# Kernel optimization log

Measured on AMD Instinct MI355X. Metric: run time of the kernel, lower is better.

Reference implementation:

```python
import jax, jax.numpy as jnp
import numpy as np

N_EMBD = 1024
N_HEAD = 16
HEAD = N_EMBD // N_HEAD


def setup_inputs() -> dict:
    key = jax.random.key(0)
    ks = jax.random.split(key, 5)
    B, T = 2, 2048
    s = 1.0 / np.sqrt(N_EMBD)
    return {
        "x": jax.random.normal(ks[0], (B, T, N_EMBD), jnp.float32),
        "w_attn": jax.random.normal(ks[1], (N_EMBD, 3 * N_EMBD), jnp.float32) * s,
        "b_attn": jnp.zeros((3 * N_EMBD,), jnp.float32),
        "w_proj": jax.random.normal(ks[2], (N_EMBD, N_EMBD), jnp.float32) * s,
        "b_proj": jnp.zeros((N_EMBD,), jnp.float32),
    }


def reference(x, w_attn, b_attn, w_proj, b_proj):
    B, T, C = x.shape
    qkv = x @ w_attn + b_attn                      # [B,T,3C]
    q, k, v = jnp.split(qkv, 3, axis=-1)
    def heads(t):
        return t.reshape(B, T, N_HEAD, HEAD).transpose(0, 2, 1, 3)  # [B,H,T,D]
    q, k, v = heads(q), heads(k), heads(v)
    scale = 1.0 / np.sqrt(HEAD)
    att = jnp.einsum('bhqd,bhkd->bhqk', q, k) * scale
    causal = jnp.tril(jnp.ones((T, T), bool))
    att = jnp.where(causal, att, -jnp.inf)
    p = jax.nn.softmax(att, axis=-1)
    y = jnp.einsum('bhqk,bhkd->bhqd', p, v)        # [B,H,T,D]
    y = y.transpose(0, 2, 1, 3).reshape(B, T, C)
    return y @ w_proj + b_proj
```

## Files before the change

### kernel.cpp

```cpp
#include <hip/hip_runtime.h>
#include <hip/hip_bf16.h>

typedef __attribute__((ext_vector_type(4))) float f32x4;
typedef __attribute__((ext_vector_type(16))) float f32x16;
typedef __attribute__((ext_vector_type(8))) short bf16x8;
typedef __attribute__((ext_vector_type(4))) unsigned int u32x4;

#define MFMA16(a,b,c) __builtin_amdgcn_mfma_f32_16x16x32_bf16(a,b,c,0,0,0)
#define MFMA32(a,b,c) __builtin_amdgcn_mfma_f32_32x32x16_bf16(a,b,c,0,0,0)
#define LOG2E 1.44269504088896340736f

__device__ __forceinline__ float bf2f(unsigned short u){
  unsigned v = ((unsigned)u) << 16;
  float f; __builtin_memcpy(&f, &v, 4); return f;
}
__device__ __forceinline__ unsigned short f2bf(float f){
  unsigned x; __builtin_memcpy(&x, &f, 4);
  x += 0x7fffu + ((x >> 16) & 1u);
  return (unsigned short)(x >> 16);
}
__device__ __forceinline__ void gload_lds16(const void* g, void* l){
  __builtin_amdgcn_global_load_lds((const __attribute__((address_space(1))) void*)g,
                                   (__attribute__((address_space(3))) void*)l, 16, 0, 0);
}
__device__ __forceinline__ f32x16 zero16(){
  f32x16 z;
#pragma unroll
  for (int i = 0; i < 16; ++i) z[i] = 0.f;
  return z;
}
__device__ __forceinline__ unsigned cvtpk(float lo, float hi_){
  unsigned d;
  asm("v_cvt_pk_bf16_f32 %0, %1, %2" : "=v"(d) : "v"(lo), "v"(hi_));
  return d;
}
__device__ __forceinline__ void pack_group(const float* p, bf16x8& f0, bf16x8& f1){
  unsigned a0 = cvtpk(p[0], p[1]),  b0 = cvtpk(p[4],  p[5]);
  unsigned a1 = cvtpk(p[2], p[3]),  b1 = cvtpk(p[6],  p[7]);
  unsigned c0 = cvtpk(p[8], p[9]),  d0 = cvtpk(p[12], p[13]);
  unsigned c1 = cvtpk(p[10],p[11]), d1 = cvtpk(p[14], p[15]);
  asm("v_permlane32_swap_b32 %0, %1" : "+v"(a0), "+v"(b0));
  asm("v_permlane32_swap_b32 %0, %1" : "+v"(a1), "+v"(b1));
  asm("v_permlane32_swap_b32 %0, %1" : "+v"(c0), "+v"(d0));
  asm("v_permlane32_swap_b32 %0, %1" : "+v"(c1), "+v"(d1));
  u32x4 w0 = {a0, a1, b0, b1};
  u32x4 w1 = {c0, c1, d0, d1};
  f0 = __builtin_bit_cast(bf16x8, w0);
  f1 = __builtin_bit_cast(bf16x8, w1);
}

__global__ void k_cast(const float* __restrict__ src, unsigned short* __restrict__ dst){
  const int i = blockIdx.x * 256 + threadIdx.x;
  const float4 v = ((const float4*)src)[i];
  ushort4 o;
  o.x = f2bf(v.x); o.y = f2bf(v.y); o.z = f2bf(v.z); o.w = f2bf(v.w);
  ((ushort4*)dst)[i] = o;
}

__global__ void k_castT(const float* __restrict__ src, unsigned short* __restrict__ dst,
                        const int R, const int C){
  __shared__ unsigned short t[64][65];
  const int r0 = blockIdx.y * 64, c0 = blockIdx.x * 64;
  const int tid = threadIdx.x;
#pragma unroll
  for (int i = 0; i < 16; ++i){
    int idx = i*256 + tid; int r = idx >> 6, c = idx & 63;
    t[r][c] = f2bf(src[(size_t)(r0 + r)*C + c0 + c]);
  }
  __syncthreads();
#pragma unroll
  for (int i = 0; i < 16; ++i){
    int idx = i*256 + tid; int c = idx >> 6, r = idx & 63;
    dst[(size_t)(c0 + c)*R + r0 + r] = t[r][c];
  }
}

__device__ __forceinline__ void gemm_core3(const unsigned short* __restrict__ A,
                                           const unsigned short* __restrict__ Bt,
                                           const int K, const int bm, const int bn,
                                           char* ldsb, f32x4 acc[4][4])
{
  const int tid = threadIdx.x, lane = tid & 63, wave = tid >> 6;
  const int wr = wave >> 1, wc = wave & 1;
  const int l15 = lane & 15, lg = lane >> 4;
  const int o = tid * 16;
  const int srow = o >> 6;
  const int sch = ((o >> 4) & 3) ^ ((srow >> 1) & 3);
  const unsigned short* gA0 = A  + (size_t)(bm + srow)*K      + sch*8;
  const unsigned short* gA1 = A  + (size_t)(bm + 64 + srow)*K + sch*8;
  const unsigned short* gB0 = Bt + (size_t)(bn + srow)*K      + sch*8;
  const unsigned short* gB1 = Bt + (size_t)(bn + 64 + srow)*K + sch*8;
  const int rsw = (l15 >> 1) & 3;
  const int aoff = (wr*64 + l15)*64 + ((lg ^ rsw) << 4);
  const int boff = 8192 + (wc*64 + l15)*64 + ((lg ^ rsw) << 4);

#define STG3(koff, bb) do { \
    gload_lds16(gA0 + (koff), ldsb + (bb) + o); \
    gload_lds16(gA1 + (koff), ldsb + (bb) + 4096 + o); \
    gload_lds16(gB0 + (koff), ldsb + (bb) + 8192 + o); \
    gload_lds16(gB1 + (koff), ldsb + (bb) + 12288 + o); } while(0)

  const int NT = K >> 5;
  STG3(0, 0);
  STG3(32, 16384);
  int bcur = 0, bstg = 32768;
  for (int t = 0; t < NT; ++t){
    if (t + 1 < NT) asm volatile("s_waitcnt vmcnt(4)" ::: "memory");
    else            asm volatile("s_waitcnt vmcnt(0)" ::: "memory");
    __builtin_amdgcn_s_barrier();
    __builtin_amdgcn_sched_barrier(0);
    if (t + 2 < NT) STG3((size_t)(t + 2) << 5, bstg);
    bf16x8 af[4], bg[4];
#pragma unroll
    for (int m = 0; m < 4; ++m) af[m] = *(const bf16x8*)(ldsb + bcur + aoff + m*1024);
#pragma unroll
    for (int n = 0; n < 4; ++n) bg[n] = *(const bf16x8*)(ldsb + bcur + boff + n*1024);
    __builtin_amdgcn_s_setprio(1);
#pragma unroll
    for (int m = 0; m < 4; ++m)
#pragma unroll
      for (int n = 0; n < 4; ++n)
        acc[m][n] = MFMA16(af[m], bg[n], acc[m][n]);
    __builtin_amdgcn_s_setprio(0);
    bcur = (bcur == 32768) ? 0 : bcur + 16384;
    bstg = (bstg == 32768) ? 0 : bstg + 16384;
  }
#undef STG3
}

__global__ __launch_bounds__(256,3) void k_gemm_qkv(const unsigned short* __restrict__ xb,
    const unsigned short* __restrict__ waT, const float* __restrict__ b_attn,
    unsigned short* __restrict__ qb, unsigned short* __restrict__ kb,
    unsigned short* __restrict__ vb)
{
  __shared__ char lds[49152];
  f32x4 acc[4][4];
#pragma unroll
  for (int m = 0; m < 4; ++m)
#pragma unroll
    for (int n = 0; n < 4; ++n) acc[m][n] = (f32x4){0.f,0.f,0.f,0.f};
  int wgid = blockIdx.y * 24 + blockIdx.x;
  wgid = (wgid & 7) * 96 + (wgid >> 3);
  const int bm = (wgid / 24) * 128, bn = (wgid % 24) * 128;
  gemm_core3(xb, waT, 1024, bm, bn, lds, acc);
  const int lane = threadIdx.x & 63, wave = threadIdx.x >> 6;
  const int wr = wave >> 1, wc = wave & 1, l15 = lane & 15, lg = lane >> 4;
#pragma unroll
  for (int m = 0; m < 4; ++m){
#pragma unroll
    for (int n = 0; n < 4; ++n){
#pragma unroll
      for (int r = 0; r < 4; ++r){
        const int row = bm + wr*64 + m*16 + lg*4 + r;
        const int col = bn + wc*64 + n*16 + l15;
        const float val = acc[m][n][r] + b_attn[col];
        const int part = col >> 10, c = col & 1023;
        const int h = c >> 6, d = c & 63;
        const int b = row >> 11, t = row & 2047;
        const unsigned short u = f2bf(val);
        const size_t bhbase = (size_t)(b*16 + h)*131072;
        if (part == 0){
          qb[bhbase + (size_t)t*64 + d] = u;
        } else {
          const int tile = t >> 6, l = t & 63;
          const size_t base = bhbase + (size_t)tile*4096;
          if (part == 1) kb[base + l*64 + ((((d>>3)^(l&7))<<3) | (d&7))] = u;
          else           vb[base + d*64 + ((((l>>3)^(d&7))<<3) | (l&7))] = u;
        }
      }
    }
  }
}

__device__ __forceinline__ void gemm_core_s(const unsigned short* __restrict__ A,
                                            const unsigned short* __restrict__ Bt,
                                            const int K, const int bm, const int bn,
                                            char* ldsb, f32x4 acc[2][4])
{
  const int tid = threadIdx.x, lane = tid & 63, wave = tid >> 6;
  const int wr = wave >> 1, wc = wave & 1;
  const int l15 = lane & 15, lg = lane >> 4;
  const int o = tid * 16;
  const int srow = o >> 6;
  const int sch = ((o >> 4) & 3) ^ ((srow >> 1) & 3);
  const unsigned short* gA0 = A  + (size_t)(bm + srow)*K      + sch*8;
  const unsigned short* gB0 = Bt + (size_t)(bn + srow)*K      + sch*8;
  const unsigned short* gB1 = Bt + (size_t)(bn + 64 + srow)*K + sch*8;
  const int rsw = (l15 >> 1) & 3;
  const int aoff = (wr*32 + l15)*64 + ((lg ^ rsw) << 4);
  const int boff = 4096 + (wc*64 + l15)*64 + ((lg ^ rsw) << 4);

#define STGS(koff, bb) do { \
    gload_lds16(gA0 + (koff), ldsb + (bb) + o); \
    gload_lds16(gB0 + (koff), ldsb + (bb) + 4096 + o); \
    gload_lds16(gB1 + (koff), ldsb + (bb) + 8192 + o); } while(0)

  const int NT = K >> 5;
  STGS(0, 0);
  STGS(32, 12288);
  int bcur = 0, bstg = 24576;
  for (int t = 0; t < NT; ++t){
    if (t + 1 < NT) asm volatile("s_waitcnt vmcnt(3)" ::: "memory");
    else            asm volatile("s_waitcnt vmcnt(0)" ::: "memory");
    __builtin_amdgcn_s_barrier();
    __builtin_amdgcn_sched_barrier(0);
    if (t + 2 < NT) STGS((size_t)(t + 2) << 5, bstg);
    bf16x8 af[2], bg[4];
#pragma unroll
    for (int m = 0; m < 2; ++m) af[m] = *(const bf16x8*)(ldsb + bcur + aoff + m*1024);
#pragma unroll
    for (int n = 0; n < 4; ++n) bg[n] = *(const bf16x8*)(ldsb + bcur + boff + n*1024);
    __builtin_amdgcn_s_setprio(1);
#pragma unroll
    for (int m = 0; m < 2; ++m)
#pragma unroll
      for (int n = 0; n < 4; ++n)
        acc[m][n] = MFMA16(af[m], bg[n], acc[m][n]);
    __builtin_amdgcn_s_setprio(0);
    bcur = (bcur == 24576) ? 0 : bcur + 12288;
    bstg = (bstg == 24576) ? 0 : bstg + 12288;
  }
#undef STGS
}

__global__ __launch_bounds__(256,4) void k_gemm_proj(const unsigned short* __restrict__ yb,
    const unsigned short* __restrict__ wpT, const float* __restrict__ b_proj,
    float* __restrict__ out)
{
  __shared__ char lds[36864];
  f32x4 acc[2][4];
#pragma unroll
  for (int m = 0; m < 2; ++m)
#pragma unroll
    for (int n = 0; n < 4; ++n) acc[m][n] = (f32x4){0.f,0.f,0.f,0.f};
  int wgid = blockIdx.y * 8 + blockIdx.x;
  wgid = (wgid & 7) * 64 + (wgid >> 3);
  const int bm = (wgid / 8) * 64, bn = (wgid % 8) * 128;
  gemm_core_s(yb, wpT, 1024, bm, bn, lds, acc);
  const int lane = threadIdx.x & 63, wave = threadIdx.x >> 6;
  const int wr = wave >> 1, wc = wave & 1, l15 = lane & 15, lg = lane >> 4;
#pragma unroll
  for (int m = 0; m < 2; ++m){
#pragma unroll
    for (int n = 0; n < 4; ++n){
#pragma unroll
      for (int r = 0; r < 4; ++r){
        const int row = bm + wr*32 + m*16 + lg*4 + r;
        const int col = bn + wc*64 + n*16 + l15;
        out[(size_t)row*1024 + col] = acc[m][n][r] + b_proj[col];
      }
    }
  }
}

__global__ __launch_bounds__(256,2) void k_attn(const unsigned short* __restrict__ q,
                       const unsigned short* __restrict__ kt,
                       const unsigned short* __restrict__ vt,
                       unsigned short* __restrict__ y)
{
  __shared__ char lds[32768];
  const int tid = threadIdx.x, lane = tid & 63, wave = tid >> 6;
  const int l31 = lane & 31, hi = lane >> 5;
  const int i = blockIdx.x, ii = i & 255;
  const int bh = ii & 31;
  const int qbi = (i < 256) ? (15 - (ii >> 5)) : (ii >> 5);
  const int q0w = qbi*128 + wave*32;
  const int ntiles = (qbi + 1) * 2;
  const unsigned short* qh = q + (size_t)bh * 131072;
  const char* kbase = (const char*)(kt + (size_t)bh * 131072);
  const char* vbase = (const char*)(vt + (size_t)bh * 131072);

  const float C = 0.125f * LOG2E;
  const float M = 16.0f;

  bf16x8 qf[4];
  {
    const unsigned short* qp = qh + (size_t)(q0w + l31)*64 + hi*8;
#pragma unroll
    for (int ds = 0; ds < 4; ++ds) qf[ds] = *(const bf16x8*)(qp + ds*16);
  }

  f32x16 yac0 = zero16(), yac1 = zero16();
  float lsum = 0.f;
  const int mask_from = q0w >> 6;
  const int stg = tid * 16;
  const int dst = wave * 1024;
  char* ldsK = lds;
  char* ldsV = lds + 16384;

#define STAGE(tile, buf) do { \
    const char* ks_ = kbase + (size_t)(tile)*8192; \
    const char* vs_ = vbase + (size_t)(tile)*8192; \
    gload_lds16(ks_ + stg,        ldsK + (buf)*8192 + dst); \
    gload_lds16(ks_ + 4096 + stg, ldsK + (buf)*8192 + 4096 + dst); \
    gload_lds16(vs_ + stg,        ldsV + (buf)*8192 + dst); \
    gload_lds16(vs_ + 4096 + stg, ldsV + (buf)*8192 + 4096 + dst); \
  } while(0)

  STAGE(0, 0);
  __syncthreads();

  const int swz = (l31 & 7) << 4;
  const int rowb = l31 * 128;

  for (int t = 0; t < ntiles; ++t){
    const int buf = t & 1;
    if (t + 1 < ntiles) STAGE(t + 1, buf ^ 1);

    const char* kb_ = ldsK + buf*8192;
    const char* vb_ = ldsV + buf*8192;

    bf16x8 kf[8];
#pragma unroll
    for (int ds = 0; ds < 4; ++ds){
      const int ch = ((ds*2 + hi) << 4) ^ swz;
      kf[ds]   = *(const bf16x8*)(kb_ + rowb + ch);
      kf[ds+4] = *(const bf16x8*)(kb_ + 4096 + rowb + ch);
    }
    f32x16 s0 = zero16(), s1 = zero16();
#pragma unroll
    for (int ds = 0; ds < 4; ++ds){
      s0 = MFMA32(kf[ds],   qf[ds], s0);
      s1 = MFMA32(kf[ds+4], qf[ds], s1);
    }

    bf16x8 vf[8];
#pragma unroll
    for (int ks = 0; ks < 4; ++ks){
      const int ch = ((ks*2 + hi) << 4) ^ swz;
      vf[ks]   = *(const bf16x8*)(vb_ + rowb + ch);
      vf[ks+4] = *(const bf16x8*)(vb_ + 4096 + rowb + ch);
    }

    if (t >= mask_from){
      const int qg = q0w + l31, key0 = t << 6;
#pragma unroll
      for (int r = 0; r < 16; ++r){
        const int kl = (r&3) + 8*(r>>2) + 4*hi;
        if (key0 + kl      > qg) s0[r] = -1e30f;
        if (key0 + 32 + kl > qg) s1[r] = -1e30f;
      }
    }

    float p0[16], p1[16];
    float ts = 0.f;
#pragma unroll
    for (int r = 0; r < 16; ++r){
      p0[r] = __builtin_amdgcn_exp2f(__builtin_fmaf(s0[r], C, -M));
      p1[r] = __builtin_amdgcn_exp2f(__builtin_fmaf(s1[r], C, -M));
      ts += p0[r] + p1[r];
    }
    lsum += ts;

    bf16x8 pa[4];
    pack_group(p0, pa[0], pa[1]);
    pack_group(p1, pa[2], pa[3]);
#pragma unroll
    for (int ks = 0; ks < 4; ++ks){
      yac0 = MFMA32(pa[ks], vf[ks],   yac0);
      yac1 = MFMA32(pa[ks], vf[ks+4], yac1);
    }
    __syncthreads();
  }
#undef STAGE

  lsum += __shfl_xor(lsum, 32);
  const float linv = 1.0f / lsum;
  const int b = bh >> 4, h = bh & 15;
  unsigned short* yp = y + ((size_t)b*2048 + q0w)*1024 + h*64;
#pragma unroll
  for (int r = 0; r < 16; ++r){
    const int ql = (r&3) + 8*(r>>2) + 4*hi;
    const float li = __shfl(linv, ql);
    yp[(size_t)ql*1024 + l31]      = f2bf(yac0[r] * li);
    yp[(size_t)ql*1024 + 32 + l31] = f2bf(yac1[r] * li);
  }
}

extern "C" void kernel_launch(void* const* d_in, const int* in_sizes, int n_in,
                              void* d_out, int out_size, void* d_ws, size_t ws_size,
                              hipStream_t stream) {
  const float* x      = (const float*)d_in[0];
  const float* w_attn = (const float*)d_in[1];
  const float* b_attn = (const float*)d_in[2];
  const float* w_proj = (const float*)d_in[3];
  const float* b_proj = (const float*)d_in[4];
  float* out = (float*)d_out;

  unsigned short* ws  = (unsigned short*)d_ws;
  unsigned short* xb  = ws;
  unsigned short* waT = xb  + 4194304;
  unsigned short* wpT = waT + 3145728;
  unsigned short* qb  = wpT + 1048576;
  unsigned short* kb  = qb  + 4194304;
  unsigned short* vb  = kb  + 4194304;
  unsigned short* yb  = vb  + 4194304;

  k_cast<<<dim3(4096), dim3(256), 0, stream>>>(x, xb);
  k_castT<<<dim3(48,16), dim3(256), 0, stream>>>(w_attn, waT, 1024, 3072);
  k_castT<<<dim3(16,16), dim3(256), 0, stream>>>(w_proj, wpT, 1024, 1024);
  k_gemm_qkv<<<dim3(24,32), dim3(256), 0, stream>>>(xb, waT, b_attn, qb, kb, vb);
  k_attn<<<dim3(512), dim3(256), 0, stream>>>(qb, kb, vb, yb);
  k_gemm_proj<<<dim3(8,64), dim3(256), 0, stream>>>(yb, wpT, b_proj, out);
}
```

Measured before the change: 101.6 us.

## Fuse x fp32-to-bf16 cast into QKV GEMM and merge weight transposes

Drops the standalone x cast kernel. The QKV GEMM now loads fp32 x tiles into registers, converts them to bf16 and writes them into a double-buffered LDS A region, while B is still staged with direct global-to-LDS loads. The two weight cast-transpose launches become one combined launch, and the block-to-tile mapping is reordered per XCD. This removes one launch and a round trip of x through the workspace, at the cost of register-path loads and extra waits inside the GEMM main loop.

Result: faster. 95.39 us (-6.1%).

```diff
diff --git a/kernel.cpp b/kernel.cpp
--- a/kernel.cpp
+++ b/kernel.cpp
@@ -49,18 +49,12 @@
   f1 = __builtin_bit_cast(bf16x8, w1);
 }
 
-__global__ void k_cast(const float* __restrict__ src, unsigned short* __restrict__ dst){
-  const int i = blockIdx.x * 256 + threadIdx.x;
-  const float4 v = ((const float4*)src)[i];
-  ushort4 o;
-  o.x = f2bf(v.x); o.y = f2bf(v.y); o.z = f2bf(v.z); o.w = f2bf(v.w);
-  ((ushort4*)dst)[i] = o;
-}
-
-__global__ void k_castT(const float* __restrict__ src, unsigned short* __restrict__ dst,
-                        const int R, const int C){
+__device__ __forceinline__ void castT_body(const float* __restrict__ src,
+                                           unsigned short* __restrict__ dst,
+                                           const int R, const int C,
+                                           const int bx, const int by){
   __shared__ unsigned short t[64][65];
-  const int r0 = blockIdx.y * 64, c0 = blockIdx.x * 64;
+  const int r0 = by * 64, c0 = bx * 64;
   const int tid = threadIdx.x;
 #pragma unroll
   for (int i = 0; i < 16; ++i){
@@ -74,77 +68,108 @@
     dst[(size_t)(c0 + c)*R + r0 + r] = t[r][c];
   }
 }
-
-__device__ __forceinline__ void gemm_core3(const unsigned short* __restrict__ A,
-                                           const unsigned short* __restrict__ Bt,
-                                           const int K, const int bm, const int bn,
-                                           char* ldsb, f32x4 acc[4][4])
-{
-  const int tid = threadIdx.x, lane = tid & 63, wave = tid >> 6;
-  const int wr = wave >> 1, wc = wave & 1;
-  const int l15 = lane & 15, lg = lane >> 4;
-  const int o = tid * 16;
-  const int srow = o >> 6;
-  const int sch = ((o >> 4) & 3) ^ ((srow >> 1) & 3);
-  const unsigned short* gA0 = A  + (size_t)(bm + srow)*K      + sch*8;
-  const unsigned short* gA1 = A  + (size_t)(bm + 64 + srow)*K + sch*8;
-  const unsigned short* gB0 = Bt + (size_t)(bn + srow)*K      + sch*8;
-  const unsigned short* gB1 = Bt + (size_t)(bn + 64 + srow)*K + sch*8;
-  const int rsw = (l15 >> 1) & 3;
-  const int aoff = (wr*64 + l15)*64 + ((lg ^ rsw) << 4);
-  const int boff = 8192 + (wc*64 + l15)*64 + ((lg ^ rsw) << 4);
-
-#define STG3(koff, bb) do { \
-    gload_lds16(gA0 + (koff), ldsb + (bb) + o); \
-    gload_lds16(gA1 + (koff), ldsb + (bb) + 4096 + o); \
-    gload_lds16(gB0 + (koff), ldsb + (bb) + 8192 + o); \
-    gload_lds16(gB1 + (koff), ldsb + (bb) + 12288 + o); } while(0)
-
-  const int NT = K >> 5;
-  STG3(0, 0);
-  STG3(32, 16384);
-  int bcur = 0, bstg = 32768;
-  for (int t = 0; t < NT; ++t){
-    if (t + 1 < NT) asm volatile("s_waitcnt vmcnt(4)" ::: "memory");
-    else            asm volatile("s_waitcnt vmcnt(0)" ::: "memory");
-    __builtin_amdgcn_s_barrier();
-    __builtin_amdgcn_sched_barrier(0);
-    if (t + 2 < NT) STG3((size_t)(t + 2) << 5, bstg);
-    bf16x8 af[4], bg[4];
-#pragma unroll
-    for (int m = 0; m < 4; ++m) af[m] = *(const bf16x8*)(ldsb + bcur + aoff + m*1024);
-#pragma unroll
-    for (int n = 0; n < 4; ++n) bg[n] = *(const bf16x8*)(ldsb + bcur + boff + n*1024);
-    __builtin_amdgcn_s_setprio(1);
-#pragma unroll
-    for (int m = 0; m < 4; ++m)
-#pragma unroll
-      for (int n = 0; n < 4; ++n)
-        acc[m][n] = MFMA16(af[m], bg[n], acc[m][n]);
-    __builtin_amdgcn_s_setprio(0);
-    bcur = (bcur == 32768) ? 0 : bcur + 16384;
-    bstg = (bstg == 32768) ? 0 : bstg + 16384;
-  }
-#undef STG3
-}
-
-__global__ __launch_bounds__(256,3) void k_gemm_qkv(const unsigned short* __restrict__ xb,
+__global__ void k_prep(const float* __restrict__ wa, const float* __restrict__ wp,
+                       unsigned short* __restrict__ waT, unsigned short* __restrict__ wpT){
+  const int bx = blockIdx.x;
+  if (bx < 48) castT_body(wa, waT, 1024, 3072, bx,      blockIdx.y);
+  else         castT_body(wp, wpT, 1024, 1024, bx - 48, blockIdx.y);
+}
+
+__global__ __launch_bounds__(256,3) void k_gemm_qkv(const float* __restrict__ x,
     const unsigned short* __restrict__ waT, const float* __restrict__ b_attn,
     unsigned short* __restrict__ qb, unsigned short* __restrict__ kb,
     unsigned short* __restrict__ vb)
 {
-  __shared__ char lds[49152];
+  __shared__ char lds[40960];
+  const int K = 1024, NT = 32;
+  const int tid = threadIdx.x, lane = tid & 63, wave = tid >> 6;
+  const int wr = wave >> 1, wc = wave & 1;
+  const int l15 = lane & 15, lg = lane >> 4;
+  char* const ldsb = (char*)lds;
+
   f32x4 acc[4][4];
 #pragma unroll
   for (int m = 0; m < 4; ++m)
 #pragma unroll
     for (int n = 0; n < 4; ++n) acc[m][n] = (f32x4){0.f,0.f,0.f,0.f};
-  int wgid = blockIdx.y * 24 + blockIdx.x;
-  wgid = (wgid & 7) * 96 + (wgid >> 3);
-  const int bm = (wgid / 24) * 128, bn = (wgid % 24) * 128;
-  gemm_core3(xb, waT, 1024, bm, bn, lds, acc);
-  const int lane = threadIdx.x & 63, wave = threadIdx.x >> 6;
-  const int wr = wave >> 1, wc = wave & 1, l15 = lane & 15, lg = lane >> 4;
+
+  const int hh0 = blockIdx.y * 24 + blockIdx.x;
+  const int xcd = hh0 & 7, idx = hh0 >> 3;
+  const int bm = (((xcd >> 1) << 3) + (idx & 7)) * 128;
+  const int bn = ((xcd & 1) * 12 + (idx >> 3)) * 128;
+
+  const int o = tid * 16;
+  const int srow = o >> 6;
+  const int sch = ((o >> 4) & 3) ^ ((srow >> 1) & 3);
+  const float* gAf0 = x + (size_t)(bm + srow)*K      + sch*8;
+  const float* gAf1 = x + (size_t)(bm + 64 + srow)*K + sch*8;
+  const unsigned short* gB0 = waT + (size_t)(bn + srow)*K      + sch*8;
+  const unsigned short* gB1 = waT + (size_t)(bn + 64 + srow)*K + sch*8;
+  const int rsw = (l15 >> 1) & 3;
+  const int aoff = (wr*64 + l15)*64 + ((lg ^ rsw) << 4);
+  const int boff = (wc*64 + l15)*64 + ((lg ^ rsw) << 4);
+
+  f32x4 aw[4];
+
+#define ALOAD(T) do{ \
+    aw[0] = *(const f32x4*)(gAf0 + (size_t)(T)*32); \
+    aw[1] = *(const f32x4*)(gAf0 + (size_t)(T)*32 + 4); \
+    aw[2] = *(const f32x4*)(gAf1 + (size_t)(T)*32); \
+    aw[3] = *(const f32x4*)(gAf1 + (size_t)(T)*32 + 4); }while(0)
+#define AWRITE(dstoff) do{ \
+    u32x4 w0_ = { cvtpk(aw[0][0],aw[0][1]), cvtpk(aw[0][2],aw[0][3]), \
+                  cvtpk(aw[1][0],aw[1][1]), cvtpk(aw[1][2],aw[1][3]) }; \
+    u32x4 w1_ = { cvtpk(aw[2][0],aw[2][1]), cvtpk(aw[2][2],aw[2][3]), \
+                  cvtpk(aw[3][0],aw[3][1]), cvtpk(aw[3][2],aw[3][3]) }; \
+    *(u32x4*)(ldsb + (dstoff) + o) = w0_; \
+    *(u32x4*)(ldsb + (dstoff) + 4096 + o) = w1_; }while(0)
+#define BSTG(T, bb) do{ \
+    gload_lds16(gB0 + (size_t)(T)*32, ldsb + 16384 + (bb) + o); \
+    gload_lds16(gB1 + (size_t)(T)*32, ldsb + 16384 + (bb) + 4096 + o); }while(0)
+
+  ALOAD(0);
+  BSTG(0, 0);
+  BSTG(1, 8192);
+  asm volatile("s_waitcnt vmcnt(4)" ::: "memory");
+  AWRITE(0);
+  asm volatile("s_waitcnt vmcnt(2)" ::: "memory");
+  asm volatile("s_waitcnt lgkmcnt(0)" ::: "memory");
+
+  int abufc = 0;
+  int bbufc = 0, bstg = 16384;
+  for (int t = 0; t < NT; ++t){
+    __builtin_amdgcn_s_barrier();
+    __builtin_amdgcn_sched_barrier(0);
+    if (t + 1 < NT) ALOAD(t + 1);
+    if (t + 2 < NT) BSTG(t + 2, bstg);
+    bf16x8 af[4], bg[4];
+#pragma unroll
+    for (int m = 0; m < 4; ++m) af[m] = *(const bf16x8*)(ldsb + abufc + aoff + m*1024);
+#pragma unroll
+    for (int n = 0; n < 4; ++n) bg[n] = *(const bf16x8*)(ldsb + 16384 + bbufc + boff + n*1024);
+    __builtin_amdgcn_s_setprio(1);
+#pragma unroll
+    for (int m = 0; m < 4; ++m)
+#pragma unroll
+      for (int n = 0; n < 4; ++n)
+        acc[m][n] = MFMA16(af[m], bg[n], acc[m][n]);
+    __builtin_amdgcn_s_setprio(0);
+    if (t + 2 < NT){
+      asm volatile("s_waitcnt vmcnt(2)" ::: "memory");
+      AWRITE(abufc ^ 8192);
+    } else if (t + 1 < NT){
+      asm volatile("s_waitcnt vmcnt(0)" ::: "memory");
+      AWRITE(abufc ^ 8192);
+    }
+    asm volatile("s_waitcnt lgkmcnt(0)" ::: "memory");
+    abufc ^= 8192;
+    bbufc = (bbufc == 16384) ? 0 : bbufc + 8192;
+    bstg  = (bstg  == 16384) ? 0 : bstg  + 8192;
+  }
+#undef ALOAD
+#undef AWRITE
+#undef BSTG
+
 #pragma unroll
   for (int m = 0; m < 4; ++m){
 #pragma unroll
@@ -388,18 +413,15 @@
   float* out = (float*)d_out;
 
   unsigned short* ws  = (unsigned short*)d_ws;
-  unsigned short* xb  = ws;
-  unsigned short* waT = xb  + 4194304;
+  unsigned short* waT = ws;
   unsigned short* wpT = waT + 3145728;
   unsigned short* qb  = wpT + 1048576;
   unsigned short* kb  = qb  + 4194304;
   unsigned short* vb  = kb  + 4194304;
   unsigned short* yb  = vb  + 4194304;
 
-  k_cast<<<dim3(4096), dim3(256), 0, stream>>>(x, xb);
-  k_castT<<<dim3(48,16), dim3(256), 0, stream>>>(w_attn, waT, 1024, 3072);
-  k_castT<<<dim3(16,16), dim3(256), 0, stream>>>(w_proj, wpT, 1024, 1024);
-  k_gemm_qkv<<<dim3(24,32), dim3(256), 0, stream>>>(xb, waT, b_attn, qb, kb, vb);
+  k_prep<<<dim3(64,16), dim3(256), 0, stream>>>(w_attn, w_proj, waT, wpT);
+  k_gemm_qkv<<<dim3(24,32), dim3(256), 0, stream>>>(x, waT, b_attn, qb, kb, vb);
   k_attn<<<dim3(512), dim3(256), 0, stream>>>(qb, kb, vb, yb);
   k_gemm_proj<<<dim3(8,64), dim3(256), 0, stream>>>(yb, wpT, b_proj, out);
 }
```
